# Kernel tuning notes

Measured on AMD Instinct MI355X. Metric: run time of the kernel, lower is better.

## Reference

```python
import jax, jax.numpy as jnp
import numpy as np

B, S, E, H = 4, 4096, 256, 2048
EPS = 1e-5

def layernorm(x, g, b):
    mu = jnp.mean(x, axis=-1, keepdims=True)
    var = jnp.mean(jnp.square(x - mu), axis=-1, keepdims=True)
    return (x - mu) * jax.lax.rsqrt(var + EPS) * g + b

def setup_inputs() -> dict:
    key = jax.random.key(0)
    ks = jax.random.split(key, 16)
    sE = 1.0 / np.sqrt(E)
    sH = 1.0 / np.sqrt(H)
    return {
        "x_embeddings": jax.random.normal(ks[0], (B, S, E), dtype=jnp.float32),
        "wq": jax.random.normal(ks[1], (E, E), dtype=jnp.float32) * sE,
        "bq": jnp.zeros((E,), jnp.float32),
        "wk": jax.random.normal(ks[2], (E, E), dtype=jnp.float32) * sE,
        "bk": jnp.zeros((E,), jnp.float32),
        "wv": jax.random.normal(ks[3], (E, E), dtype=jnp.float32) * sE,
        "bv": jnp.zeros((E,), jnp.float32),
        "w0": jax.random.normal(ks[4], (E, E), dtype=jnp.float32) * sE,
        "b0": jnp.zeros((E,), jnp.float32),
        "w1": jax.random.normal(ks[5], (E, H), dtype=jnp.float32) * sE,
        "b1": jnp.zeros((H,), jnp.float32),
        "ln_mlp_g": jnp.ones((H,), jnp.float32),
        "ln_mlp_b": jnp.zeros((H,), jnp.float32),
        "w2": jax.random.normal(ks[6], (H, E), dtype=jnp.float32) * sH,
        "b2": jnp.zeros((E,), jnp.float32),
        "ln1_g": jnp.ones((E,), jnp.float32),
        "ln1_b": jnp.zeros((E,), jnp.float32),
        "ln2_g": jnp.ones((E,), jnp.float32),
        "ln2_b": jnp.zeros((E,), jnp.float32),
    }

def reference(x_embeddings, wq, bq, wk, bk, wv, bv, w0, b0,
              w1, b1, ln_mlp_g, ln_mlp_b, w2, b2,
              ln1_g, ln1_b, ln2_g, ln2_b):
    x = x_embeddings
    q = x @ wq + bq
    k = x @ wk + bk
    v = x @ wv + bv
    # Unscaled, unmasked attention (faithful to source: no 1/sqrt(d), mask unused)
    scores = jnp.einsum('bqd,bkd->bqk', q, k)          # [B,S,S]
    probs = jax.nn.softmax(scores, axis=-1)
    attn = jnp.einsum('bqk,bkd->bqd', probs, v)        # [B,S,E]
    e = layernorm(x + attn, ln1_g, ln1_b) @ w0 + b0
    h = e @ w1 + b1                                     # [B,S,H]
    h = jax.nn.leaky_relu(layernorm(h, ln_mlp_g, ln_mlp_b))  # LnActivation: LN + LeakyReLU
    logits = h @ w2 + b2                                # [B,S,E]
    return layernorm(jax.nn.leaky_relu(logits + e), ln2_g, ln2_b)
```

## Files before the change

kernel.cpp:

```cpp
#include <hip/hip_runtime.h>

typedef unsigned short u16;
typedef unsigned int   u32;
typedef u16   u16x4 __attribute__((ext_vector_type(4)));
typedef u16   u16x8 __attribute__((ext_vector_type(8)));
typedef short s16x8 __attribute__((ext_vector_type(8)));
typedef u32   u32x4 __attribute__((ext_vector_type(4)));
typedef float f32x4 __attribute__((ext_vector_type(4)));
typedef _Float16 f16x8 __attribute__((ext_vector_type(8)));

__device__ __forceinline__ u16 f2b(float f) {
  u32 u = __builtin_bit_cast(u32, f);
  u32 r = (u + 0x7fffu + ((u >> 16) & 1u)) >> 16;
  return (u16)r;
}
__device__ __forceinline__ float b2f(u16 h) {
  return __builtin_bit_cast(float, (u32)h << 16);
}
__device__ __forceinline__ u16 f2h(float f) {
  _Float16 h = (_Float16)f;
  return __builtin_bit_cast(u16, h);
}
__device__ __forceinline__ u32 cvtpk(float a, float b) {
  u32 r; asm("v_cvt_pk_bf16_f32 %0, %1, %2" : "=v"(r) : "v"(a), "v"(b)); return r;
}

__device__ __forceinline__ void async16(void* l, const void* g) {
  __builtin_amdgcn_global_load_lds((const __attribute__((address_space(1))) u32*)g,
                                   (__attribute__((address_space(3))) u32*)l, 16, 0, 0);
}

__device__ __forceinline__ float wave_sum(float v) {
#pragma unroll
  for (int m = 32; m; m >>= 1) v += __shfl_xor(v, m, 64);
  return v;
}

constexpr int BM = 128, BN = 128, BK = 64;

template<bool SPLIT, int OMODE>
__global__ __launch_bounds__(256)
void k_gemm_bt(const u16* __restrict__ Ah, const u16* __restrict__ Al, long lda,
               const u16* __restrict__ Bh, const u16* __restrict__ Bl, long ldb,
               const float* __restrict__ bias,
               float* __restrict__ Cf, u16* __restrict__ Cb, u16* __restrict__ Cl,
               long ldc, int K)
{
  __shared__ u16 lds[(SPLIT ? 4 : 2) * BM * BK];
  const int tid = threadIdx.x;
  const long arow0 = (long)blockIdx.y * BM;
  const long bcol0 = (long)blockIdx.x * BN;

  long offA[4], offB[4];
#pragma unroll
  for (int r = 0; r < 4; ++r) {
    const int off = r * 4096 + tid * 16;
    const int row = off >> 7;
    const int colb = off & 127;
    offA[r] = (arow0 + row) * lda + (colb >> 1);
    offB[r] = (bcol0 + row) * ldb + (colb >> 1);
  }

  const int lane = tid & 63;
  const int wid = tid >> 6;
  const int wr = (wid >> 1) * 64;
  const int wc = (wid & 1) * 64;
  const int fr = lane & 15;
  const int fk = (lane >> 4) * 8;

  f32x4 acc[4][4] = {};

  for (int k0 = 0; k0 < K; k0 += BK) {
#pragma unroll
    for (int r = 0; r < 4; ++r) {
      const int loff = (r * 4096 + tid * 16) >> 1;
      async16(&lds[loff],           Ah + offA[r] + k0);
      async16(&lds[BM*BK + loff],   Bh + offB[r] + k0);
      if constexpr (SPLIT) {
        async16(&lds[2*BM*BK + loff], Al + offA[r] + k0);
        async16(&lds[3*BM*BK + loff], Bl + offB[r] + k0);
      }
    }
    __syncthreads();
#pragma unroll
    for (int kk = 0; kk < BK; kk += 32) {
      s16x8 a[4], b[4];
#pragma unroll
      for (int m = 0; m < 4; ++m)
        a[m] = *(const s16x8*)&lds[(wr + m*16 + fr) * BK + kk + fk];
#pragma unroll
      for (int n = 0; n < 4; ++n)
        b[n] = *(const s16x8*)&lds[BM*BK + (wc + n*16 + fr) * BK + kk + fk];
#pragma unroll
      for (int m = 0; m < 4; ++m)
#pragma unroll
        for (int n = 0; n < 4; ++n)
          acc[m][n] = __builtin_amdgcn_mfma_f32_16x16x32_bf16(a[m], b[n], acc[m][n], 0, 0, 0);
      if constexpr (SPLIT) {
        s16x8 al[4], bl[4];
#pragma unroll
        for (int m = 0; m < 4; ++m)
          al[m] = *(const s16x8*)&lds[2*BM*BK + (wr + m*16 + fr) * BK + kk + fk];
#pragma unroll
        for (int n = 0; n < 4; ++n)
          bl[n] = *(const s16x8*)&lds[3*BM*BK + (wc + n*16 + fr) * BK + kk + fk];
#pragma unroll
        for (int m = 0; m < 4; ++m)
#pragma unroll
          for (int n = 0; n < 4; ++n) {
            acc[m][n] = __builtin_amdgcn_mfma_f32_16x16x32_bf16(a[m], bl[n], acc[m][n], 0, 0, 0);
            acc[m][n] = __builtin_amdgcn_mfma_f32_16x16x32_bf16(al[m], b[n], acc[m][n], 0, 0, 0);
          }
      }
    }
    __syncthreads();
  }

  float bv[4];
#pragma unroll
  for (int n = 0; n < 4; ++n) {
    const long gcol = bcol0 + wc + n*16 + fr;
    bv[n] = bias ? bias[gcol] : 0.f;
  }

#pragma unroll
  for (int m = 0; m < 4; ++m) {
#pragma unroll
    for (int reg = 0; reg < 4; ++reg) {
      const long grow = arow0 + wr + m*16 + (lane >> 4) * 4 + reg;
      const long ro = grow * ldc;
#pragma unroll
      for (int n = 0; n < 4; ++n) {
        const long gcol = bcol0 + wc + n*16 + fr;
        const float val = acc[m][n][reg] + bv[n];
        if constexpr (OMODE == 0) {
          Cf[ro + gcol] = val;
        } else {
          Cb[ro + gcol] = f2b(val);
        }
      }
    }
  }
}

__global__ __launch_bounds__(256)
void k_gemm_qkv(const float* __restrict__ Af,
                const u16* __restrict__ Bh, const u16* __restrict__ Bl,
                const float* __restrict__ bias,
                u16* __restrict__ Cq, u16* __restrict__ Ck, u16* __restrict__ Cv)
{
  __shared__ float ldsA[BM * BK];
  __shared__ u16 ldsBh[BN * BK];
  __shared__ u16 ldsBl[BN * BK];
  const int tid = threadIdx.x;
  const long arow0 = (long)blockIdx.y * BM;
  const long bcol0 = (long)blockIdx.x * BN;

  long offA[8];
#pragma unroll
  for (int r = 0; r < 8; ++r) {
    const int off = r * 4096 + tid * 16;
    const int row = off >> 8;
    const int colb = off & 255;
    offA[r] = (arow0 + row) * 256 + (colb >> 2);
  }
  long offB[4];
#pragma unroll
  for (int r = 0; r < 4; ++r) {
    const int off = r * 4096 + tid * 16;
    const int row = off >> 7;
    const int colb = off & 127;
    offB[r] = (bcol0 + row) * 256 + (colb >> 1);
  }

  const int lane = tid & 63;
  const int wid = tid >> 6;
  const int wr = (wid >> 1) * 64;
  const int wc = (wid & 1) * 64;
  const int fr = lane & 15;
  const int fk = (lane >> 4) * 8;

  f32x4 acc[4][4] = {};

  for (int k0 = 0; k0 < 256; k0 += BK) {
#pragma unroll
    for (int r = 0; r < 8; ++r)
      async16((char*)ldsA + r*4096 + tid*16, Af + offA[r] + k0);
#pragma unroll
    for (int r = 0; r < 4; ++r) {
      const int loff = (r * 4096 + tid * 16) >> 1;
      async16(&ldsBh[loff], Bh + offB[r] + k0);
      async16(&ldsBl[loff], Bl + offB[r] + k0);
    }
    __syncthreads();
#pragma unroll
    for (int kk = 0; kk < BK; kk += 32) {
      s16x8 a[4], al[4];
#pragma unroll
      for (int m = 0; m < 4; ++m) {
        const float* ap = &ldsA[(wr + m*16 + fr) * BK + kk + fk];
        const float4 v0 = *(const float4*)ap;
        const float4 v1 = *(const float4*)(ap + 4);
        u32x4 H, L;
        H[0] = cvtpk(v0.x, v0.y); H[1] = cvtpk(v0.z, v0.w);
        H[2] = cvtpk(v1.x, v1.y); H[3] = cvtpk(v1.z, v1.w);
        L[0] = cvtpk(v0.x - __builtin_bit_cast(float, H[0] << 16),
                     v0.y - __builtin_bit_cast(float, H[0] & 0xffff0000u));
        L[1] = cvtpk(v0.z - __builtin_bit_cast(float, H[1] << 16),
                     v0.w - __builtin_bit_cast(float, H[1] & 0xffff0000u));
        L[2] = cvtpk(v1.x - __builtin_bit_cast(float, H[2] << 16),
                     v1.y - __builtin_bit_cast(float, H[2] & 0xffff0000u));
        L[3] = cvtpk(v1.z - __builtin_bit_cast(float, H[3] << 16),
                     v1.w - __builtin_bit_cast(float, H[3] & 0xffff0000u));
        a[m]  = __builtin_bit_cast(s16x8, H);
        al[m] = __builtin_bit_cast(s16x8, L);
      }
      s16x8 b[4], bl[4];
#pragma unroll
      for (int n = 0; n < 4; ++n) {
        b[n]  = *(const s16x8*)&ldsBh[(wc + n*16 + fr) * BK + kk + fk];
        bl[n] = *(const s16x8*)&ldsBl[(wc + n*16 + fr) * BK + kk + fk];
      }
#pragma unroll
      for (int m = 0; m < 4; ++m)
#pragma unroll
        for (int n = 0; n < 4; ++n) {
          acc[m][n] = __builtin_amdgcn_mfma_f32_16x16x32_bf16(a[m],  b[n],  acc[m][n], 0, 0, 0);
          acc[m][n] = __builtin_amdgcn_mfma_f32_16x16x32_bf16(a[m],  bl[n], acc[m][n], 0, 0, 0);
          acc[m][n] = __builtin_amdgcn_mfma_f32_16x16x32_bf16(al[m], b[n],  acc[m][n], 0, 0, 0);
        }
    }
    __syncthreads();
  }

  float bv[4];
#pragma unroll
  for (int n = 0; n < 4; ++n)
    bv[n] = bias[bcol0 + wc + n*16 + fr];

  const int band = (int)(bcol0 >> 8);
  u16* dst = (band == 0) ? Cq : (band == 1) ? Ck : Cv;

#pragma unroll
  for (int m = 0; m < 4; ++m) {
#pragma unroll
    for (int reg = 0; reg < 4; ++reg) {
      const long grow = arow0 + wr + m*16 + (lane >> 4) * 4 + reg;
#pragma unroll
      for (int n = 0; n < 4; ++n) {
        const long lc = bcol0 - (long)band*256 + wc + n*16 + fr;
        const float val = acc[m][n][reg] + bv[n];
        dst[grow * 256 + lc] = (band < 2) ? f2h(val) : f2b(val);
      }
    }
  }
}

__global__ __launch_bounds__(256)
void k_flash(const u16* __restrict__ q16, const u16* __restrict__ k16,
             const u16* __restrict__ vt,
             const float* __restrict__ x,
             const float* __restrict__ g, const float* __restrict__ b,
             u16* __restrict__ ln1)
{
  __shared__ u16 lkh[2][64*256];
  __shared__ float lS[32*68];
  __shared__ u16 lP[32*72];
  __shared__ float lm[32], ll[32], lsc[32];

  const int tid = threadIdx.x;
  const int lane = tid & 63, wid = tid >> 6;
  const long bo = (long)blockIdx.y * 1048576;
  const long q0 = (long)blockIdx.x * 32;

  const int fr  = lane & 15;
  const int hi2 = lane >> 4;
  const int fk  = hi2 * 8;
  const int qh_sel = wid >> 1;
  const int kh_sel = wid & 1;

  f16x8 qf[8];
  {
    const u16* qp = q16 + bo + (q0 + qh_sel*16 + fr) * 256;
#pragma unroll
    for (int c = 0; c < 8; ++c)
      qf[c] = *(const f16x8*)(qp + c*32 + fk);
  }

  if (tid < 32) { lm[tid] = -1e30f; ll[tid] = 0.f; }
  f32x4 acc[2][4] = {};

  const char* kp = (const char*)(k16 + bo);
  const u16* vbase = vt + bo;

  auto STAGE = [&](int k0s, int bsel) {
#pragma unroll
    for (int r = 0; r < 8; ++r) {
      const int L = r*4096 + tid*16;
      const int row = L >> 9;
      const int colb = L & 511;
      const long gb = (long)(k0s + row)*512 + (colb ^ ((row & 7) << 4));
      async16((char*)lkh[bsel] + L, kp + gb);
    }
  };

  STAGE(0, 0);
  __syncthreads();

  int cur = 0;
  for (int k0 = 0; k0 < 4096; k0 += 64) {
    s16x8 vb[2][4];
#pragma unroll
    for (int ks = 0; ks < 2; ++ks)
#pragma unroll
      for (int j = 0; j < 4; ++j)
        vb[ks][j] = *(const s16x8*)(vbase + (long)(wid*64 + j*16 + fr)*4096 + k0 + ks*32 + fk);

    if (k0 + 64 < 4096) STAGE(k0 + 64, cur ^ 1);

    f32x4 s0 = {}, s1 = {};
    const int kc0 = kh_sel*32 + fr;
    const int swz = (kc0 & 7) << 4;
#pragma unroll
    for (int c = 0; c < 8; ++c) {
      const int o = (c*64 + hi2*16) ^ swz;
      const f16x8 b0 = *(const f16x8*)((const char*)lkh[cur] + kc0*512 + o);
      const f16x8 b1 = *(const f16x8*)((const char*)lkh[cur] + (kc0 + 16)*512 + o);
      s0 = __builtin_amdgcn_mfma_f32_16x16x32_f16(qf[c], b0, s0, 0, 0, 0);
      s1 = __builtin_amdgcn_mfma_f32_16x16x32_f16(qf[c], b1, s1, 0, 0, 0);
    }
#pragma unroll
    for (int r = 0; r < 4; ++r) {
      const int srow = (qh_sel*16 + hi2*4 + r) * 68;
      lS[srow + kh_sel*32 + fr]      = s0[r];
      lS[srow + kh_sel*32 + 16 + fr] = s1[r];
    }
    __syncthreads();

    {
      const int sr = tid >> 3;
      const int sc = (tid & 7) * 8;
      const float4 sv0 = *(const float4*)&lS[sr*68 + sc];
      const float4 sv1 = *(const float4*)&lS[sr*68 + sc + 4];
      float tmx = fmaxf(fmaxf(fmaxf(sv0.x, sv0.y), fmaxf(sv0.z, sv0.w)),
                        fmaxf(fmaxf(sv1.x, sv1.y), fmaxf(sv1.z, sv1.w)));
#pragma unroll
      for (int m = 1; m < 8; m <<= 1) tmx = fmaxf(tmx, __shfl_xor(tmx, m, 64));
      const float mold = lm[sr];
      const float mnew = fmaxf(mold, tmx);
      const float p0 = __expf(sv0.x - mnew), p1 = __expf(sv0.y - mnew);
      const float p2 = __expf(sv0.z - mnew), p3 = __expf(sv0.w - mnew);
      const float p4 = __expf(sv1.x - mnew), p5 = __expf(sv1.y - mnew);
      const float p6 = __expf(sv1.z - mnew), p7 = __expf(sv1.w - mnew);
      float ps = ((p0 + p1) + (p2 + p3)) + ((p4 + p5) + (p6 + p7));
#pragma unroll
      for (int m = 1; m < 8; m <<= 1) ps += __shfl_xor(ps, m, 64);
      const float scale = __expf(mold - mnew);
      if ((tid & 7) == 0) {
        lm[sr] = mnew;
        ll[sr] = ll[sr] * scale + ps;
        lsc[sr] = scale;
      }
      u16x8 pb;
      pb[0]=f2b(p0); pb[1]=f2b(p1); pb[2]=f2b(p2); pb[3]=f2b(p3);
      pb[4]=f2b(p4); pb[5]=f2b(p5); pb[6]=f2b(p6); pb[7]=f2b(p7);
      *(u16x8*)&lP[sr*72 + sc] = pb;
    }
    __syncthreads();

#pragma unroll
    for (int qm = 0; qm < 2; ++qm)
#pragma unroll
      for (int r = 0; r < 4; ++r) {
        const float s = lsc[qm*16 + hi2*4 + r];
#pragma unroll
        for (int j = 0; j < 4; ++j) acc[qm][j][r] *= s;
      }
#pragma unroll
    for (int qm = 0; qm < 2; ++qm)
#pragma unroll
      for (int ks = 0; ks < 2; ++ks) {
        const s16x8 pa = *(const s16x8*)&lP[(qm*16 + fr)*72 + ks*32 + fk];
#pragma unroll
        for (int j = 0; j < 4; ++j)
          acc[qm][j] = __builtin_amdgcn_mfma_f32_16x16x32_bf16(pa, vb[ks][j], acc[qm][j], 0, 0, 0);
      }
    cur ^= 1;
  }

  __syncthreads();
  float gv4[4], bv4[4];
#pragma unroll
  for (int j = 0; j < 4; ++j) {
    gv4[j] = g[wid*64 + j*16 + fr];
    bv4[j] = b[wid*64 + j*16 + fr];
  }
  const float* xb = x + bo + q0*256;
#pragma unroll
  for (int qm = 0; qm < 2; ++qm)
#pragma unroll
    for (int r = 0; r < 4; ++r) {
      const int row = qm*16 + hi2*4 + r;
      const float inv = 1.0f / ll[row];
      const float* xp = xb + (long)row*256 + wid*64 + fr;
      float s = 0.f, qq = 0.f;
#pragma unroll
      for (int j = 0; j < 4; ++j) {
        const float t = acc[qm][j][r] * inv + xp[j*16];
        acc[qm][j][r] = t;
        s += t; qq += t*t;
      }
#pragma unroll
      for (int m = 1; m < 16; m <<= 1) {
        s  += __shfl_xor(s, m, 64);
        qq += __shfl_xor(qq, m, 64);
      }
      if (fr == 0) { lS[row*4 + wid] = s; lS[128 + row*4 + wid] = qq; }
    }
  __syncthreads();
#pragma unroll
  for (int qm = 0; qm < 2; ++qm)
#pragma unroll
    for (int r = 0; r < 4; ++r) {
      const int row = qm*16 + hi2*4 + r;
      const float s  = (lS[row*4+0] + lS[row*4+1]) + (lS[row*4+2] + lS[row*4+3]);
      const float qq = (lS[128+row*4+0] + lS[128+row*4+1]) + (lS[128+row*4+2] + lS[128+row*4+3]);
      const float mu = s * (1.f / 256.f);
      const float var = qq * (1.f / 256.f) - mu * mu;
      const float rs = rsqrtf(var + 1e-5f);
      u16* op = ln1 + bo + (q0 + row)*256 + wid*64 + fr;
#pragma unroll
      for (int j = 0; j < 4; ++j)
        op[j*16] = f2b((acc[qm][j][r] - mu) * rs * gv4[j] + bv4[j]);
    }
}


__global__ __launch_bounds__(256)
void k_transpose_qkv0(const float* __restrict__ wq, const float* __restrict__ wk,
                      const float* __restrict__ wv, const float* __restrict__ w0,
                      u16* __restrict__ catT_h, u16* __restrict__ catT_l,
                      u16* __restrict__ w0T,
                      const float* __restrict__ bq, const float* __restrict__ bk,
                      const float* __restrict__ bv, float* __restrict__ catBias) {
  __shared__ float t[32][33];
  const int z = blockIdx.z;
  const float* in = (z == 0) ? wq : (z == 1) ? wk : (z == 2) ? wv : w0;
  const int c0 = blockIdx.x * 32, r0 = blockIdx.y * 32;
  const int tx = threadIdx.x, ty = threadIdx.y;
#pragma unroll
  for (int i = 0; i < 4; ++i)
    t[ty + i*8][tx] = in[(long)(r0 + ty + i*8) * 256 + c0 + tx];
  __syncthreads();
#pragma unroll
  for (int i = 0; i < 4; ++i) {
    const float f = t[tx][ty + i*8];
    const u16 hb = f2b(f);
    if (z < 3) {
      const long o = (long)(z*256 + c0 + ty + i*8) * 256 + r0 + tx;
      catT_h[o] = hb;
      catT_l[o] = f2b(f - b2f(hb));
    } else {
      w0T[(long)(c0 + ty + i*8) * 256 + r0 + tx] = hb;
    }
  }
  if (z == 3 && blockIdx.x == 0 && blockIdx.y == 0) {
    const int t0 = ty * 32 + tx;
    catBias[t0] = bq[t0];
    catBias[256 + t0] = bk[t0];
    catBias[512 + t0] = bv[t0];
  }
}

__global__ __launch_bounds__(256)
void k_transpose_f32ns(const float* __restrict__ in, u16* __restrict__ hi, int R, int C) {
  __shared__ float t[32][33];
  const int c0 = blockIdx.x * 32, r0 = blockIdx.y * 32;
  const int tx = threadIdx.x, ty = threadIdx.y;
#pragma unroll
  for (int i = 0; i < 4; ++i)
    t[ty + i*8][tx] = in[(long)(r0 + ty + i*8) * C + c0 + tx];
  __syncthreads();
#pragma unroll
  for (int i = 0; i < 4; ++i)
    hi[(long)(c0 + ty + i*8) * R + r0 + tx] = f2b(t[tx][ty + i*8]);
}

__global__ __launch_bounds__(256)
void k_transpose_bf16(const u16* __restrict__ in, u16* __restrict__ out,
                      int R, int C, long sIn, long sOut) {
  __shared__ u16 t[32][34];
  const int z = blockIdx.z;
  const u16* ib = in + (long)z * sIn;
  u16* ob = out + (long)z * sOut;
  const int c0 = blockIdx.x * 32, r0 = blockIdx.y * 32;
  const int tx = threadIdx.x, ty = threadIdx.y;
#pragma unroll
  for (int i = 0; i < 4; ++i)
    t[ty + i*8][tx] = ib[(long)(r0 + ty + i*8) * C + c0 + tx];
  __syncthreads();
#pragma unroll
  for (int i = 0; i < 4; ++i)
    ob[(long)(c0 + ty + i*8) * R + r0 + tx] = t[tx][ty + i*8];
}

__global__ __launch_bounds__(256)
void k_ln_leaky(const u16* __restrict__ h, const float* __restrict__ g,
                const float* __restrict__ b, u16* __restrict__ out) {
  const long row = blockIdx.x;
  const int tid = threadIdx.x;
  const int lane = tid & 63, wid = tid >> 6;
  const u16x8 hv = *(const u16x8*)(h + row * 2048 + tid * 8);
  float f[8];
  float s = 0.f, q = 0.f;
#pragma unroll
  for (int j = 0; j < 8; ++j) { f[j] = b2f(hv[j]); s += f[j]; q += f[j] * f[j]; }
  s = wave_sum(s); q = wave_sum(q);
  __shared__ float rs_[4], rq_[4];
  if (lane == 0) { rs_[wid] = s; rq_[wid] = q; }
  __syncthreads();
  s = rs_[0] + rs_[1] + rs_[2] + rs_[3];
  q = rq_[0] + rq_[1] + rq_[2] + rq_[3];
  const float mu = s * (1.f / 2048.f);
  const float var = q * (1.f / 2048.f) - mu * mu;
  const float rsq = rsqrtf(var + 1e-5f);
  const float4 g0 = *(const float4*)(g + tid * 8);
  const float4 g1 = *(const float4*)(g + tid * 8 + 4);
  const float4 b0 = *(const float4*)(b + tid * 8);
  const float4 b1 = *(const float4*)(b + tid * 8 + 4);
  const float gg[8] = {g0.x, g0.y, g0.z, g0.w, g1.x, g1.y, g1.z, g1.w};
  const float bb[8] = {b0.x, b0.y, b0.z, b0.w, b1.x, b1.y, b1.z, b1.w};
  u16x8 o;
#pragma unroll
  for (int j = 0; j < 8; ++j) {
    float y = (f[j] - mu) * rsq * gg[j] + bb[j];
    y = y > 0.f ? y : 0.01f * y;
    o[j] = f2b(y);
  }
  *(u16x8*)(out + row * 2048 + tid * 8) = o;
}

__global__ __launch_bounds__(256)
void k_final(const float* __restrict__ lg, const u16* __restrict__ e,
             const float* __restrict__ g, const float* __restrict__ b,
             float* __restrict__ out) {
  const long row = (long)blockIdx.x * 4 + (threadIdx.x >> 6);
  const int lane = threadIdx.x & 63;
  const long base = row * 256 + lane * 4;
  const float4 lv = *(const float4*)(lg + base);
  const u16x4 ev = *(const u16x4*)(e + base);
  float t[4] = {lv.x + b2f(ev[0]), lv.y + b2f(ev[1]), lv.z + b2f(ev[2]), lv.w + b2f(ev[3])};
#pragma unroll
  for (int j = 0; j < 4; ++j) t[j] = t[j] > 0.f ? t[j] : 0.01f * t[j];
  float s = t[0] + t[1] + t[2] + t[3];
  float q = t[0]*t[0] + t[1]*t[1] + t[2]*t[2] + t[3]*t[3];
  s = wave_sum(s); q = wave_sum(q);
  const float mu = s * (1.f / 256.f);
  const float var = q * (1.f / 256.f) - mu * mu;
  const float rs = rsqrtf(var + 1e-5f);
  const float4 gv = *(const float4*)(g + lane * 4);
  const float4 bv = *(const float4*)(b + lane * 4);
  float4 o;
  o.x = (t[0] - mu) * rs * gv.x + bv.x;
  o.y = (t[1] - mu) * rs * gv.y + bv.y;
  o.z = (t[2] - mu) * rs * gv.z + bv.z;
  o.w = (t[3] - mu) * rs * gv.w + bv.w;
  *(float4*)(out + base) = o;
}


extern "C" void kernel_launch(void* const* d_in, const int* in_sizes, int n_in,
                              void* d_out, int out_size, void* d_ws, size_t ws_size,
                              hipStream_t stream) {
  const float* x   = (const float*)d_in[0];
  const float* wq  = (const float*)d_in[1];
  const float* bq  = (const float*)d_in[2];
  const float* wk  = (const float*)d_in[3];
  const float* bk  = (const float*)d_in[4];
  const float* wv  = (const float*)d_in[5];
  const float* bv_ = (const float*)d_in[6];
  const float* w0  = (const float*)d_in[7];
  const float* b0  = (const float*)d_in[8];
  const float* w1  = (const float*)d_in[9];
  const float* b1  = (const float*)d_in[10];
  const float* lmg = (const float*)d_in[11];
  const float* lmb = (const float*)d_in[12];
  const float* w2  = (const float*)d_in[13];
  const float* b2  = (const float*)d_in[14];
  const float* l1g = (const float*)d_in[15];
  const float* l1b = (const float*)d_in[16];
  const float* l2g = (const float*)d_in[17];
  const float* l2b = (const float*)d_in[18];

  char* ws = (char*)d_ws;
  float* out = (float*)d_out;

  u16* q16    = (u16*)(ws + 0);
  u16* k16    = (u16*)(ws + 16777216);
  u16* vT     = (u16*)(ws + 33554432);
  u16* v_b    = (u16*)(ws + 58720256);
  u16* ln1    = (u16*)(ws + 75497472);
  u16* e_b    = (u16*)(ws + 83886080);
  float* logits = (float*)(ws + 92274688);
  u16* h_b    = (u16*)(ws + 0);
  u16* catT_h = (u16*)(ws + 109051904);
  u16* catT_l = (u16*)(ws + 109445120);
  u16* w0T    = (u16*)(ws + 109838336);
  u16* w1T    = (u16*)(ws + 109969408);
  u16* w2T    = (u16*)(ws + 111017984);
  float* catBias = (float*)(ws + 112066560);

  const dim3 t256(256);
  const dim3 tr(32, 8);

  k_transpose_qkv0<<<dim3(8, 8, 4), tr, 0, stream>>>(
      wq, wk, wv, w0, catT_h, catT_l, w0T, bq, bk, bv_, catBias);
  k_transpose_f32ns<<<dim3(64, 8), tr, 0, stream>>>(w1, w1T, 256, 2048);
  k_transpose_f32ns<<<dim3(8, 64), tr, 0, stream>>>(w2, w2T, 2048, 256);

  k_gemm_qkv<<<dim3(6, 128), t256, 0, stream>>>(
      x, catT_h, catT_l, catBias, q16, k16, v_b);
  k_transpose_bf16<<<dim3(8, 128, 4), tr, 0, stream>>>(v_b, vT, 4096, 256, 1048576, 1048576);

  k_flash<<<dim3(128, 4), t256, 0, stream>>>(q16, k16, vT, x, l1g, l1b, ln1);

  k_gemm_bt<false, 1><<<dim3(2, 128), t256, 0, stream>>>(
      ln1, nullptr, 256, w0T, nullptr, 256, b0, nullptr, e_b, nullptr, 256, 256);
  k_gemm_bt<false, 1><<<dim3(16, 128), t256, 0, stream>>>(
      e_b, nullptr, 256, w1T, nullptr, 256, b1, nullptr, h_b, nullptr, 2048, 256);
  k_ln_leaky<<<16384, t256, 0, stream>>>(h_b, lmg, lmb, h_b);
  k_gemm_bt<false, 0><<<dim3(2, 128), t256, 0, stream>>>(
      h_b, nullptr, 2048, w2T, nullptr, 2048, b2, logits, nullptr, nullptr, 256, 2048);
  k_final<<<4096, t256, 0, stream>>>(logits, e_b, l2g, l2b, out);
}
```

Baseline: 334.0 us.

## Fuse MLP layernorm stats into W1 GEMM epilogue and apply LN+leaky in W2 prologue

The W1 GEMM now emits per-row partial sums and sums of squares while storing h, a small kernel reduces them to mean and rsqrt, and the W2 GEMM normalizes and applies leaky ReLU to A tiles as it loads them into LDS. This removes the standalone LN pass, which read and wrote the full 16384x2048 bf16 hidden tensor. The cost is that the W2 GEMM's A path switches from async copies to synchronous register loads plus ALU work. Statistics are computed from unrounded fp32 values rather than the bf16-rounded h, which slightly changes numerics.

```diff
diff --git a/kernel.cpp b/kernel.cpp
--- a/kernel.cpp
+++ b/kernel.cpp
@@ -138,6 +138,210 @@
         } else {
           Cb[ro + gcol] = f2b(val);
         }
+      }
+    }
+  }
+}
+
+__global__ __launch_bounds__(256)
+void k_gemm_h(const u16* __restrict__ Ah, const u16* __restrict__ Bh,
+              const float* __restrict__ bias, u16* __restrict__ Cb,
+              float* __restrict__ pS, float* __restrict__ pQ)
+{
+  __shared__ u16 lds[2 * BM * BK];
+  const int tid = threadIdx.x;
+  const long arow0 = (long)blockIdx.y * BM;
+  const long bcol0 = (long)blockIdx.x * BN;
+
+  long offA[4], offB[4];
+#pragma unroll
+  for (int r = 0; r < 4; ++r) {
+    const int off = r * 4096 + tid * 16;
+    const int row = off >> 7;
+    const int colb = off & 127;
+    offA[r] = (arow0 + row) * 256 + (colb >> 1);
+    offB[r] = (bcol0 + row) * 256 + (colb >> 1);
+  }
+
+  const int lane = tid & 63;
+  const int wid = tid >> 6;
+  const int wr = (wid >> 1) * 64;
+  const int wc = (wid & 1) * 64;
+  const int fr = lane & 15;
+  const int fk = (lane >> 4) * 8;
+
+  f32x4 acc[4][4] = {};
+
+  for (int k0 = 0; k0 < 256; k0 += BK) {
+#pragma unroll
+    for (int r = 0; r < 4; ++r) {
+      const int loff = (r * 4096 + tid * 16) >> 1;
+      async16(&lds[loff],         Ah + offA[r] + k0);
+      async16(&lds[BM*BK + loff], Bh + offB[r] + k0);
+    }
+    __syncthreads();
+#pragma unroll
+    for (int kk = 0; kk < BK; kk += 32) {
+      s16x8 a[4], b[4];
+#pragma unroll
+      for (int m = 0; m < 4; ++m)
+        a[m] = *(const s16x8*)&lds[(wr + m*16 + fr) * BK + kk + fk];
+#pragma unroll
+      for (int n = 0; n < 4; ++n)
+        b[n] = *(const s16x8*)&lds[BM*BK + (wc + n*16 + fr) * BK + kk + fk];
+#pragma unroll
+      for (int m = 0; m < 4; ++m)
+#pragma unroll
+        for (int n = 0; n < 4; ++n)
+          acc[m][n] = __builtin_amdgcn_mfma_f32_16x16x32_bf16(a[m], b[n], acc[m][n], 0, 0, 0);
+    }
+    __syncthreads();
+  }
+
+  float bv[4];
+#pragma unroll
+  for (int n = 0; n < 4; ++n)
+    bv[n] = bias[bcol0 + wc + n*16 + fr];
+
+  const int slot = blockIdx.x * 2 + (wid & 1);
+#pragma unroll
+  for (int m = 0; m < 4; ++m) {
+#pragma unroll
+    for (int reg = 0; reg < 4; ++reg) {
+      const long grow = arow0 + wr + m*16 + (lane >> 4) * 4 + reg;
+      const long ro = grow * 2048;
+      float s = 0.f, q = 0.f;
+#pragma unroll
+      for (int n = 0; n < 4; ++n) {
+        const long gcol = bcol0 + wc + n*16 + fr;
+        const float val = acc[m][n][reg] + bv[n];
+        Cb[ro + gcol] = f2b(val);
+        s += val; q += val * val;
+      }
+#pragma unroll
+      for (int msk = 1; msk < 16; msk <<= 1) {
+        s += __shfl_xor(s, msk, 64);
+        q += __shfl_xor(q, msk, 64);
+      }
+      if ((lane & 15) == 0) {
+        pS[(long)slot * 16384 + grow] = s;
+        pQ[(long)slot * 16384 + grow] = q;
+      }
+    }
+  }
+}
+
+__global__ __launch_bounds__(256)
+void k_ln_stats(const float* __restrict__ pS, const float* __restrict__ pQ,
+                float* __restrict__ smu, float* __restrict__ srs)
+{
+  const long row = (long)blockIdx.x * 256 + threadIdx.x;
+  float s = 0.f, q = 0.f;
+#pragma unroll
+  for (int i = 0; i < 32; ++i) {
+    s += pS[(long)i * 16384 + row];
+    q += pQ[(long)i * 16384 + row];
+  }
+  const float mu = s * (1.f / 2048.f);
+  const float var = q * (1.f / 2048.f) - mu * mu;
+  smu[row] = mu;
+  srs[row] = rsqrtf(var + 1e-5f);
+}
+
+__global__ __launch_bounds__(256)
+void k_gemm_w2(const u16* __restrict__ Ah, const float* __restrict__ smu,
+               const float* __restrict__ srs, const float* __restrict__ lg,
+               const float* __restrict__ lb, const u16* __restrict__ Bh,
+               const float* __restrict__ bias, float* __restrict__ Cf)
+{
+  __shared__ u16 ldsA[BM * BK];
+  __shared__ u16 ldsB[BN * BK];
+  const int tid = threadIdx.x;
+  const long arow0 = (long)blockIdx.y * BM;
+  const long bcol0 = (long)blockIdx.x * BN;
+
+  int arow[4]; int acol[4];
+  float mu4[4], rs4[4];
+#pragma unroll
+  for (int r = 0; r < 4; ++r) {
+    const int off = r * 4096 + tid * 16;
+    arow[r] = off >> 7;
+    acol[r] = (off & 127) >> 1;
+    mu4[r] = smu[arow0 + arow[r]];
+    rs4[r] = srs[arow0 + arow[r]];
+  }
+  long offB[4];
+#pragma unroll
+  for (int r = 0; r < 4; ++r) {
+    const int off = r * 4096 + tid * 16;
+    offB[r] = (bcol0 + (off >> 7)) * 2048 + ((off & 127) >> 1);
+  }
+
+  const int lane = tid & 63;
+  const int wid = tid >> 6;
+  const int wr = (wid >> 1) * 64;
+  const int wc = (wid & 1) * 64;
+  const int fr = lane & 15;
+  const int fk = (lane >> 4) * 8;
+
+  f32x4 acc[4][4] = {};
+
+  for (int k0 = 0; k0 < 2048; k0 += BK) {
+#pragma unroll
+    for (int r = 0; r < 4; ++r)
+      async16(&ldsB[(r * 4096 + tid * 16) >> 1], Bh + offB[r] + k0);
+#pragma unroll
+    for (int r = 0; r < 4; ++r) {
+      const u16x8 hv = *(const u16x8*)(Ah + (long)(arow0 + arow[r]) * 2048 + k0 + acol[r]);
+      const float4 g0 = *(const float4*)(lg + k0 + acol[r]);
+      const float4 g1 = *(const float4*)(lg + k0 + acol[r] + 4);
+      const float4 b0 = *(const float4*)(lb + k0 + acol[r]);
+      const float4 b1 = *(const float4*)(lb + k0 + acol[r] + 4);
+      const float gg[8] = {g0.x, g0.y, g0.z, g0.w, g1.x, g1.y, g1.z, g1.w};
+      const float bb[8] = {b0.x, b0.y, b0.z, b0.w, b1.x, b1.y, b1.z, b1.w};
+      u16x8 o;
+#pragma unroll
+      for (int j = 0; j < 8; ++j) {
+        float y = (b2f(hv[j]) - mu4[r]) * rs4[r] * gg[j] + bb[j];
+        y = y > 0.f ? y : 0.01f * y;
+        o[j] = f2b(y);
+      }
+      *(u16x8*)&ldsA[(r * 4096 + tid * 16) >> 1] = o;
+    }
+    __syncthreads();
+#pragma unroll
+    for (int kk = 0; kk < BK; kk += 32) {
+      s16x8 a[4], b[4];
+#pragma unroll
+      for (int m = 0; m < 4; ++m)
+        a[m] = *(const s16x8*)&ldsA[(wr + m*16 + fr) * BK + kk + fk];
+#pragma unroll
+      for (int n = 0; n < 4; ++n)
+        b[n] = *(const s16x8*)&ldsB[(wc + n*16 + fr) * BK + kk + fk];
+#pragma unroll
+      for (int m = 0; m < 4; ++m)
+#pragma unroll
+        for (int n = 0; n < 4; ++n)
+          acc[m][n] = __builtin_amdgcn_mfma_f32_16x16x32_bf16(a[m], b[n], acc[m][n], 0, 0, 0);
+    }
+    __syncthreads();
+  }
+
+  float bv[4];
+#pragma unroll
+  for (int n = 0; n < 4; ++n)
+    bv[n] = bias[bcol0 + wc + n*16 + fr];
+
+#pragma unroll
+  for (int m = 0; m < 4; ++m) {
+#pragma unroll
+    for (int reg = 0; reg < 4; ++reg) {
+      const long grow = arow0 + wr + m*16 + (lane >> 4) * 4 + reg;
+      const long ro = grow * 256;
+#pragma unroll
+      for (int n = 0; n < 4; ++n) {
+        const long gcol = bcol0 + wc + n*16 + fr;
+        Cf[ro + gcol] = acc[m][n][reg] + bv[n];
       }
     }
   }
@@ -502,42 +706,6 @@
 #pragma unroll
   for (int i = 0; i < 4; ++i)
     ob[(long)(c0 + ty + i*8) * R + r0 + tx] = t[tx][ty + i*8];
-}
-
-__global__ __launch_bounds__(256)
-void k_ln_leaky(const u16* __restrict__ h, const float* __restrict__ g,
-                const float* __restrict__ b, u16* __restrict__ out) {
-  const long row = blockIdx.x;
-  const int tid = threadIdx.x;
-  const int lane = tid & 63, wid = tid >> 6;
-  const u16x8 hv = *(const u16x8*)(h + row * 2048 + tid * 8);
-  float f[8];
-  float s = 0.f, q = 0.f;
-#pragma unroll
-  for (int j = 0; j < 8; ++j) { f[j] = b2f(hv[j]); s += f[j]; q += f[j] * f[j]; }
-  s = wave_sum(s); q = wave_sum(q);
-  __shared__ float rs_[4], rq_[4];
-  if (lane == 0) { rs_[wid] = s; rq_[wid] = q; }
-  __syncthreads();
-  s = rs_[0] + rs_[1] + rs_[2] + rs_[3];
-  q = rq_[0] + rq_[1] + rq_[2] + rq_[3];
-  const float mu = s * (1.f / 2048.f);
-  const float var = q * (1.f / 2048.f) - mu * mu;
-  const float rsq = rsqrtf(var + 1e-5f);
-  const float4 g0 = *(const float4*)(g + tid * 8);
-  const float4 g1 = *(const float4*)(g + tid * 8 + 4);
-  const float4 b0 = *(const float4*)(b + tid * 8);
-  const float4 b1 = *(const float4*)(b + tid * 8 + 4);
-  const float gg[8] = {g0.x, g0.y, g0.z, g0.w, g1.x, g1.y, g1.z, g1.w};
-  const float bb[8] = {b0.x, b0.y, b0.z, b0.w, b1.x, b1.y, b1.z, b1.w};
-  u16x8 o;
-#pragma unroll
-  for (int j = 0; j < 8; ++j) {
-    float y = (f[j] - mu) * rsq * gg[j] + bb[j];
-    y = y > 0.f ? y : 0.01f * y;
-    o[j] = f2b(y);
-  }
-  *(u16x8*)(out + row * 2048 + tid * 8) = o;
 }
 
 __global__ __launch_bounds__(256)
@@ -599,6 +767,10 @@
   u16* k16    = (u16*)(ws + 16777216);
   u16* vT     = (u16*)(ws + 33554432);
   u16* v_b    = (u16*)(ws + 58720256);
+  float* pS   = (float*)(ws + 67108864);
+  float* pQ   = (float*)(ws + 69206016);
+  float* smu  = (float*)(ws + 71303168);
+  float* srs  = (float*)(ws + 71368704);
   u16* ln1    = (u16*)(ws + 75497472);
   u16* e_b    = (u16*)(ws + 83886080);
   float* logits = (float*)(ws + 92274688);
@@ -626,10 +798,9 @@
 
   k_gemm_bt<false, 1><<<dim3(2, 128), t256, 0, stream>>>(
       ln1, nullptr, 256, w0T, nullptr, 256, b0, nullptr, e_b, nullptr, 256, 256);
-  k_gemm_bt<false, 1><<<dim3(16, 128), t256, 0, stream>>>(
-      e_b, nullptr, 256, w1T, nullptr, 256, b1, nullptr, h_b, nullptr, 2048, 256);
-  k_ln_leaky<<<16384, t256, 0, stream>>>(h_b, lmg, lmb, h_b);
-  k_gemm_bt<false, 0><<<dim3(2, 128), t256, 0, stream>>>(
-      h_b, nullptr, 2048, w2T, nullptr, 2048, b2, logits, nullptr, nullptr, 256, 2048);
+  k_gemm_h<<<dim3(16, 128), t256, 0, stream>>>(e_b, w1T, b1, h_b, pS, pQ);
+  k_ln_stats<<<64, t256, 0, stream>>>(pS, pQ, smu, srs);
+  k_gemm_w2<<<dim3(2, 128), t256, 0, stream>>>(
+      h_b, smu, srs, lmg, lmb, w2T, b2, logits);
   k_final<<<4096, t256, 0, stream>>>(logits, e_b, l2g, l2b, out);
 }
```

New measurement: 344.3 us. 1.03x slower.

## Split-K the W2 GEMM into two halves and sum partials in final LN

Applied to the files above, without the earlier changes.

Replaces the single K=2048 W2 GEMM launch (256 blocks) with a split-K kernel that launches 512 blocks, each covering half of K and writing its own fp32 partial logits buffer. The final layernorm kernel reads both partials and adds them, and the bias is applied only in the first split. This gives the GPU more blocks to fill its compute units on a long-K, narrow-N GEMM, at the cost of an extra fp32 partial buffer write and read. The new kernel also uses a simpler single-buffered load loop that may differ from the generic GEMM's pipelining.

```diff
diff --git a/kernel.cpp b/kernel.cpp
--- a/kernel.cpp
+++ b/kernel.cpp
@@ -138,6 +138,84 @@
         } else {
           Cb[ro + gcol] = f2b(val);
         }
+      }
+    }
+  }
+}
+
+__global__ __launch_bounds__(256)
+void k_gemm_w2sk(const u16* __restrict__ Ah, const u16* __restrict__ Bh,
+                 const float* __restrict__ bias,
+                 float* __restrict__ C0, float* __restrict__ C1)
+{
+  __shared__ u16 lds[2 * BM * BK];
+  const int tid = threadIdx.x;
+  const long arow0 = (long)blockIdx.y * BM;
+  const long bcol0 = (long)blockIdx.x * BN;
+  const int zs = blockIdx.z;
+  const int kbase = zs * 1024;
+  float* Cz = zs ? C1 : C0;
+
+  long offA[4], offB[4];
+#pragma unroll
+  for (int r = 0; r < 4; ++r) {
+    const int off = r * 4096 + tid * 16;
+    const int row = off >> 7;
+    const int colb = off & 127;
+    offA[r] = (arow0 + row) * 2048 + (colb >> 1) + kbase;
+    offB[r] = (bcol0 + row) * 2048 + (colb >> 1) + kbase;
+  }
+
+  const int lane = tid & 63;
+  const int wid = tid >> 6;
+  const int wr = (wid >> 1) * 64;
+  const int wc = (wid & 1) * 64;
+  const int fr = lane & 15;
+  const int fk = (lane >> 4) * 8;
+
+  f32x4 acc[4][4] = {};
+
+  for (int k0 = 0; k0 < 1024; k0 += BK) {
+#pragma unroll
+    for (int r = 0; r < 4; ++r) {
+      const int loff = (r * 4096 + tid * 16) >> 1;
+      async16(&lds[loff],         Ah + offA[r] + k0);
+      async16(&lds[BM*BK + loff], Bh + offB[r] + k0);
+    }
+    __syncthreads();
+#pragma unroll
+    for (int kk = 0; kk < BK; kk += 32) {
+      s16x8 a[4], b[4];
+#pragma unroll
+      for (int m = 0; m < 4; ++m)
+        a[m] = *(const s16x8*)&lds[(wr + m*16 + fr) * BK + kk + fk];
+#pragma unroll
+      for (int n = 0; n < 4; ++n)
+        b[n] = *(const s16x8*)&lds[BM*BK + (wc + n*16 + fr) * BK + kk + fk];
+#pragma unroll
+      for (int m = 0; m < 4; ++m)
+#pragma unroll
+        for (int n = 0; n < 4; ++n)
+          acc[m][n] = __builtin_amdgcn_mfma_f32_16x16x32_bf16(a[m], b[n], acc[m][n], 0, 0, 0);
+    }
+    __syncthreads();
+  }
+
+  float bv[4];
+#pragma unroll
+  for (int n = 0; n < 4; ++n)
+    bv[n] = (zs == 0) ? bias[bcol0 + wc + n*16 + fr] : 0.f;
+
+#pragma unroll
+  for (int m = 0; m < 4; ++m) {
+#pragma unroll
+    for (int reg = 0; reg < 4; ++reg) {
+      const long grow = arow0 + wr + m*16 + (lane >> 4) * 4 + reg;
+      const long ro = grow * 256;
+#pragma unroll
+      for (int n = 0; n < 4; ++n) {
+        const long gcol = bcol0 + wc + n*16 + fr;
+        Cz[ro + gcol] = acc[m][n][reg] + bv[n];
       }
     }
   }
@@ -541,15 +619,18 @@
 }
 
 __global__ __launch_bounds__(256)
-void k_final(const float* __restrict__ lg, const u16* __restrict__ e,
+void k_final(const float* __restrict__ lg0, const float* __restrict__ lg1,
+             const u16* __restrict__ e,
              const float* __restrict__ g, const float* __restrict__ b,
              float* __restrict__ out) {
   const long row = (long)blockIdx.x * 4 + (threadIdx.x >> 6);
   const int lane = threadIdx.x & 63;
   const long base = row * 256 + lane * 4;
-  const float4 lv = *(const float4*)(lg + base);
+  const float4 l0 = *(const float4*)(lg0 + base);
+  const float4 l1 = *(const float4*)(lg1 + base);
   const u16x4 ev = *(const u16x4*)(e + base);
-  float t[4] = {lv.x + b2f(ev[0]), lv.y + b2f(ev[1]), lv.z + b2f(ev[2]), lv.w + b2f(ev[3])};
+  float t[4] = {l0.x + l1.x + b2f(ev[0]), l0.y + l1.y + b2f(ev[1]),
+                l0.z + l1.z + b2f(ev[2]), l0.w + l1.w + b2f(ev[3])};
 #pragma unroll
   for (int j = 0; j < 4; ++j) t[j] = t[j] > 0.f ? t[j] : 0.01f * t[j];
   float s = t[0] + t[1] + t[2] + t[3];
@@ -609,6 +690,7 @@
   u16* w1T    = (u16*)(ws + 109969408);
   u16* w2T    = (u16*)(ws + 111017984);
   float* catBias = (float*)(ws + 112066560);
+  float* logits2 = (float*)(ws + 112069888);
 
   const dim3 t256(256);
   const dim3 tr(32, 8);
@@ -629,7 +711,6 @@
   k_gemm_bt<false, 1><<<dim3(16, 128), t256, 0, stream>>>(
       e_b, nullptr, 256, w1T, nullptr, 256, b1, nullptr, h_b, nullptr, 2048, 256);
   k_ln_leaky<<<16384, t256, 0, stream>>>(h_b, lmg, lmb, h_b);
-  k_gemm_bt<false, 0><<<dim3(2, 128), t256, 0, stream>>>(
-      h_b, nullptr, 2048, w2T, nullptr, 2048, b2, logits, nullptr, nullptr, 256, 2048);
-  k_final<<<4096, t256, 0, stream>>>(logits, e_b, l2g, l2b, out);
-}
+  k_gemm_w2sk<<<dim3(2, 128, 2), t256, 0, stream>>>(h_b, w2T, b2, logits, logits2);
+  k_final<<<4096, t256, 0, stream>>>(logits, logits2, e_b, l2g, l2b, out);
+}
```

Result: faster. 319.7 us (-4.3%).
